# Kernel tuning notes

Measured on AMD Instinct MI355X. Metric: run time of the kernel, lower is better.

## Reference

```python
import jax, jax.numpy as jnp
import numpy as np

B, S, D, H = 2, 2048, 1024, 16
DEPTH = D // H
NEG = -1e9


def setup_inputs() -> dict:
    key = jax.random.key(0)
    ks = jax.random.split(key, 8)
    scale = 1.0 / np.sqrt(D)
    inp = {
        "query": jax.random.normal(ks[0], (B, S, D), jnp.float32),
        "key": jax.random.normal(ks[1], (B, S, D), jnp.float32),
        "value": jax.random.normal(ks[2], (B, S, D), jnp.float32),
        # causal look-ahead mask: 1 where attention is disallowed
        "mask": (1.0 - jnp.tril(jnp.ones((S, S), jnp.float32)))[None, None, :, :],
        "Wq": jax.random.normal(ks[3], (D, D), jnp.float32) * scale,
        "Wk": jax.random.normal(ks[4], (D, D), jnp.float32) * scale,
        "Wv": jax.random.normal(ks[5], (D, D), jnp.float32) * scale,
        "Wo": jax.random.normal(ks[6], (D, D), jnp.float32) * scale,
        "bq": jnp.zeros((D,), jnp.float32),
        "bk": jnp.zeros((D,), jnp.float32),
        "bv": jnp.zeros((D,), jnp.float32),
        "bo": jnp.zeros((D,), jnp.float32),
    }
    return inp


def _split_heads(x):
    # [B,S,D] -> [B,H,S,depth]
    return x.reshape(B, -1, H, DEPTH).transpose(0, 2, 1, 3)


def reference(query, key, value, mask, Wq, Wk, Wv, Wo, bq, bk, bv, bo):
    q = _split_heads(query @ Wq + bq)
    k = _split_heads(key @ Wk + bk)
    v = _split_heads(value @ Wv + bv)
    logits = jnp.einsum("bhqd,bhkd->bhqk", q, k) / jnp.sqrt(jnp.float32(DEPTH))
    logits = logits + mask * NEG
    attn = jax.nn.softmax(logits, axis=-1)
    ctx = jnp.einsum("bhqk,bhkd->bhqd", attn, v)  # [B,H,S,depth]
    concat = ctx.transpose(0, 2, 1, 3).reshape(B, -1, D)
    return concat @ Wo + bo
```

## Files before the change

kernel.cpp:

```cpp
#include <hip/hip_runtime.h>
#include <hip/hip_bf16.h>
#include <stdint.h>

#define BB 2
#define SS 2048
#define DDIM 1024
#define HH 16
#define DEPTH 64
#define MROWS (BB*SS)

typedef short bf16x8 __attribute__((ext_vector_type(8)));
typedef float f32x4 __attribute__((ext_vector_type(4)));

__device__ inline ushort f2bf(float f) {
  union { float f; unsigned u; } v; v.f = f;
  unsigned r = v.u + 0x7fffu + ((v.u >> 16) & 1u);
  return (ushort)(r >> 16);
}

__device__ inline uint pkbf(float a, float b) {
  uint r;
  asm("v_cvt_pk_bf16_f32 %0, %1, %2" : "=v"(r) : "v"(a), "v"(b));
  return r;
}

__device__ inline void gload_lds16(const void* g, void* l) {
  __builtin_amdgcn_global_load_lds(
      (const __attribute__((address_space(1))) unsigned*)g,
      (__attribute__((address_space(3))) unsigned*)l,
      16, 0, 0);
}

__global__ void wprep_kernel(const float* __restrict__ W0, const float* __restrict__ W1,
                             const float* __restrict__ W2, const float* __restrict__ W3,
                             ushort* __restrict__ T0, ushort* __restrict__ T1,
                             ushort* __restrict__ T2, ushort* __restrict__ T3) {
  __shared__ float tile[32][33];
  int z = blockIdx.x >> 10;
  int rr = blockIdx.x & 1023;
  const float* W = (z == 0) ? W0 : (z == 1) ? W1 : (z == 2) ? W2 : W3;
  ushort* T = (z == 0) ? T0 : (z == 1) ? T1 : (z == 2) ? T2 : T3;
  int tx = threadIdx.x & 31, ty = threadIdx.x >> 5;
  int n0 = (rr & 31) * 32, k0 = (rr >> 5) * 32;
#pragma unroll
  for (int i = 0; i < 4; i++)
    tile[ty + i * 8][tx] = W[(size_t)(k0 + ty + i * 8) * DDIM + n0 + tx];
  __syncthreads();
#pragma unroll
  for (int i = 0; i < 4; i++)
    T[(size_t)(n0 + ty + i * 8) * DDIM + k0 + tx] = f2bf(tile[tx][ty + i * 8]);
}

__global__ __launch_bounds__(256, 3) void qkv_gemm_kernel(
    const float* __restrict__ Aq, const float* __restrict__ Ak, const float* __restrict__ Av,
    const ushort* __restrict__ Wqt, const ushort* __restrict__ Wkt, const ushort* __restrict__ Wvt,
    const float* __restrict__ bqp, const float* __restrict__ bkp, const float* __restrict__ bvp,
    ushort* __restrict__ Qh, ushort* __restrict__ Kh, ushort* __restrict__ Vtg) {
  const int id = blockIdx.x;
  const int xcd = id & 7;
  const int rest = id >> 3;
  const int xblk = rest & 7;
  const int slot = rest >> 3;
  const int g = xcd * 12 + slot;
  const int yblk = g & 31;
  const int z = g >> 5;

  const float*  Ap = (z == 0) ? Aq  : (z == 1) ? Ak  : Av;
  const ushort* Bt = (z == 0) ? Wqt : (z == 1) ? Wkt : Wvt;
  const float* bias = (z == 0) ? bqp : (z == 1) ? bkp : bvp;

  __shared__ __align__(16) ushort As[128 * 64];
  __shared__ __align__(16) ushort Bs[128 * 64];
  const int tid = threadIdx.x;
  const int w = tid >> 6, lane = tid & 63;
  const int m0 = yblk * 128, n0 = xblk * 128;
  const int wr = (w >> 1) * 64, wc = (w & 1) * 64;
  const int l4 = lane >> 4, l15 = lane & 15;
  const int row16 = tid >> 4;
  const int col4 = (tid & 15) * 4;
  const int srow8 = w * 8 + (lane >> 3);
  const int scol8 = (lane & 7) * 8;

  f32x4 zero = {0.f, 0.f, 0.f, 0.f};
  f32x4 acc[4][4];
#pragma unroll
  for (int i = 0; i < 4; i++)
#pragma unroll
    for (int j = 0; j < 4; j++) acc[i][j] = zero;

  float4 areg[8];
#pragma unroll
  for (int j = 0; j < 8; ++j)
    areg[j] = *(const float4*)&Ap[(size_t)(m0 + j * 16 + row16) * DDIM + col4];

  for (int t = 0; t < 16; ++t) {
#pragma unroll
    for (int it = 0; it < 4; ++it)
      gload_lds16(Bt + (size_t)(n0 + it * 32 + srow8) * DDIM + t * 64 + scol8,
                  &Bs[(it * 32 + w * 8) * 64]);
#pragma unroll
    for (int j = 0; j < 8; ++j) {
      uint2 pk;
      pk.x = pkbf(areg[j].x, areg[j].y);
      pk.y = pkbf(areg[j].z, areg[j].w);
      *(uint2*)&As[(j * 16 + row16) * 64 + col4] = pk;
    }
    __syncthreads();
    if (t + 1 < 16) {
#pragma unroll
      for (int j = 0; j < 8; ++j)
        areg[j] = *(const float4*)&Ap[(size_t)(m0 + j * 16 + row16) * DDIM + (t + 1) * 64 + col4];
    }
#pragma unroll
    for (int kk = 0; kk < 2; ++kk) {
      bf16x8 af[4], bfr[4];
#pragma unroll
      for (int m = 0; m < 4; m++)
        af[m] = *(const bf16x8*)&As[(wr + m * 16 + l15) * 64 + kk * 32 + l4 * 8];
#pragma unroll
      for (int n = 0; n < 4; n++)
        bfr[n] = *(const bf16x8*)&Bs[(wc + n * 16 + l15) * 64 + kk * 32 + l4 * 8];
#pragma unroll
      for (int m = 0; m < 4; m++)
#pragma unroll
        for (int n = 0; n < 4; n++)
          acc[m][n] = __builtin_amdgcn_mfma_f32_16x16x32_bf16(af[m], bfr[n], acc[m][n], 0, 0, 0);
    }
    __syncthreads();
  }

  if (z != 2) {
    ushort* outp = (z == 0) ? Qh : Kh;
    ushort* wtile = (w < 2) ? &As[w * 4096] : &Bs[(w - 2) * 4096];
    const int gcol0 = n0 + wc;
    const int hh = gcol0 >> 6;
    const int bb = m0 >> 11;
    const int s0g = (m0 + wr) & (SS - 1);
#pragma unroll
    for (int m = 0; m < 4; m++) {
#pragma unroll
      for (int n = 0; n < 4; n++) {
        int dloc = n * 16 + l15;
        float bv = bias[gcol0 + dloc];
#pragma unroll
        for (int r = 0; r < 4; r++) {
          int sloc = m * 16 + l4 * 4 + r;
          wtile[sloc * 64 + (dloc ^ ((sloc & 7) << 3))] = f2bf(acc[m][n][r] + bv);
        }
      }
    }
#pragma unroll
    for (int i = 0; i < 8; ++i) {
      int srow = i * 8 + (lane >> 3);
      int dch = (lane & 7) * 8;
      bf16x8 val = *(const bf16x8*)&wtile[srow * 64 + (dch ^ ((srow & 7) << 3))];
      *(bf16x8*)&outp[((size_t)(bb * HH + hh) * SS + s0g + srow) * DEPTH + dch] = val;
    }
  } else {
    ushort* wtile = (w < 2) ? &As[w * 2048] : &Bs[(w - 2) * 2048];
    const int gcol0 = n0 + wc;
    const int hh = gcol0 >> 6;
    const int bb = m0 >> 11;
    const int s0g = (m0 + wr) & (SS - 1);
#pragma unroll
    for (int p = 0; p < 2; ++p) {
#pragma unroll
      for (int nn = 0; nn < 2; ++nn) {
        int n = p * 2 + nn;
        int dloc = nn * 16 + l15;
        float bv = bias[gcol0 + p * 32 + dloc];
#pragma unroll
        for (int m = 0; m < 4; m++) {
#pragma unroll
          for (int rr = 0; rr < 4; rr += 2) {
            int sloc = m * 16 + l4 * 4 + rr;
            int gg = (sloc >> 3) ^ (dloc & 7);
            uint pk = pkbf(acc[m][n][rr] + bv, acc[m][n][rr + 1] + bv);
            *(uint*)&wtile[dloc * 64 + gg * 8 + (sloc & 7)] = pk;
          }
        }
      }
      __syncthreads();
#pragma unroll
      for (int i = 0; i < 4; ++i) {
        int dloc = (lane >> 3) + i * 8;
        int gg = (lane & 7) ^ (dloc & 7);
        bf16x8 val = *(const bf16x8*)&wtile[dloc * 64 + gg * 8];
        int dglob = p * 32 + dloc;
        size_t addr = ((size_t)(bb * HH + hh) * DEPTH + dglob) * SS + s0g + (lane & 7) * 8;
        *(bf16x8*)&Vtg[addr] = val;
      }
      __syncthreads();
    }
  }
}

__global__ __launch_bounds__(256, 2) void out_gemm_kernel(
    const ushort* __restrict__ A, const ushort* __restrict__ Bt,
    const float* __restrict__ bias, float* __restrict__ out,
    int M, int N, int K) {
  __shared__ __align__(16) ushort As[128 * 64];
  __shared__ __align__(16) ushort Bs[64 * 64];
  const int id = blockIdx.x;
  const int xcd = id & 7;
  const int rest = id >> 3;
  const int xblk = rest & 15;
  const int slot = rest >> 4;
  const int yblk = xcd * 4 + slot;

  const int tid = threadIdx.x;
  const int w = tid >> 6, lane = tid & 63;
  const int m0 = yblk * 128, n0 = xblk * 64;
  const int wr = (w >> 1) * 64, wc = (w & 1) * 32;
  const int l4 = lane >> 4, l15 = lane & 15;
  const int srow8 = w * 8 + (lane >> 3);
  const int scol8 = (lane & 7) * 8;

  f32x4 zero = {0.f, 0.f, 0.f, 0.f};
  f32x4 acc[4][2];
#pragma unroll
  for (int i = 0; i < 4; i++)
#pragma unroll
    for (int j = 0; j < 2; j++) acc[i][j] = zero;

  for (int t = 0; t < 16; ++t) {
#pragma unroll
    for (int it = 0; it < 4; ++it)
      gload_lds16(A + (size_t)(m0 + it * 32 + srow8) * K + t * 64 + scol8,
                  &As[(it * 32 + w * 8) * 64]);
#pragma unroll
    for (int it = 0; it < 2; ++it)
      gload_lds16(Bt + (size_t)(n0 + it * 32 + srow8) * K + t * 64 + scol8,
                  &Bs[(it * 32 + w * 8) * 64]);
    __syncthreads();
#pragma unroll
    for (int kk = 0; kk < 2; ++kk) {
      bf16x8 af[4], bfr[2];
#pragma unroll
      for (int m = 0; m < 4; m++)
        af[m] = *(const bf16x8*)&As[(wr + m * 16 + l15) * 64 + kk * 32 + l4 * 8];
#pragma unroll
      for (int n = 0; n < 2; n++)
        bfr[n] = *(const bf16x8*)&Bs[(wc + n * 16 + l15) * 64 + kk * 32 + l4 * 8];
#pragma unroll
      for (int m = 0; m < 4; m++)
#pragma unroll
        for (int n = 0; n < 2; n++)
          acc[m][n] = __builtin_amdgcn_mfma_f32_16x16x32_bf16(af[m], bfr[n], acc[m][n], 0, 0, 0);
    }
    __syncthreads();
  }

#pragma unroll
  for (int m = 0; m < 4; m++) {
#pragma unroll
    for (int n = 0; n < 2; n++) {
      int col = n0 + wc + n * 16 + l15;
      float bv = bias[col];
#pragma unroll
      for (int r = 0; r < 4; r++) {
        int row = m0 + wr + m * 16 + l4 * 4 + r;
        out[(size_t)row * N + col] = acc[m][n][r] + bv;
      }
    }
  }
}

__global__ __launch_bounds__(256, 4) void attn_kernel(
    const ushort* __restrict__ Qh, const ushort* __restrict__ Kh,
    const ushort* __restrict__ Vt, ushort* __restrict__ ctx) {
  __shared__ __align__(16) ushort Ks[2][64 * 64];
  __shared__ __align__(16) ushort Vs[2][64 * 64];
  __shared__ __align__(16) ushort Ps[4][16 * 64];
  const int tid = threadIdx.x;
  const int w = tid >> 6, lane = tid & 63;
  const int l4 = lane >> 4, l15 = lane & 15;
  const float CE = 0.18033688f;

  const int xcd = blockIdx.x & 7;
  const int local = blockIdx.x >> 3;
  const int bh = xcd * 4 + (local & 3);
  const int chunk = 31 - (local >> 2);
  const int b = bh >> 4, h = bh & 15;
  const size_t qkbase = (size_t)bh * SS * DEPTH;
  const size_t vbase  = (size_t)bh * DEPTH * SS;

  const int srow_w = w * 8 + (lane >> 3);
  const int colb_lin = (lane & 7) * 16;
  const int swz_rd = (l15 & 7) << 3;

  const int q0 = chunk * 64 + w * 16;
  const int nt = chunk + 1;

  bf16x8 aq[2];
#pragma unroll
  for (int cc = 0; cc < 2; cc++)
    aq[cc] = *(const bf16x8*)&Qh[qkbase + (size_t)(q0 + l15) * DEPTH + cc * 32 + l4 * 8];

  f32x4 zero = {0.f, 0.f, 0.f, 0.f};
  f32x4 o[4];
  float m_run = -__builtin_inff(), l_run = 0.f;
#pragma unroll
  for (int d = 0; d < 4; d++) o[d] = zero;

  int buf = 0;
#pragma unroll
  for (int it = 0; it < 2; ++it) {
    int row = it * 32 + srow_w;
    int col_e = (colb_lin ^ ((row & 7) << 4)) >> 1;
    int ldsoff = it * 2048 + w * 512;
    gload_lds16(Kh + qkbase + (size_t)row * DEPTH + col_e, &Ks[0][ldsoff]);
    gload_lds16(Vt + vbase + (size_t)row * SS + col_e, &Vs[0][ldsoff]);
  }
  __syncthreads();

  for (int t = 0; t < nt; ++t) {
    if (t + 1 < nt) {
      const int kv1 = (t + 1) * 64;
#pragma unroll
      for (int it = 0; it < 2; ++it) {
        int row = it * 32 + srow_w;
        int col_e = (colb_lin ^ ((row & 7) << 4)) >> 1;
        int ldsoff = it * 2048 + w * 512;
        gload_lds16(Kh + qkbase + (size_t)(kv1 + row) * DEPTH + col_e, &Ks[buf ^ 1][ldsoff]);
        gload_lds16(Vt + vbase + (size_t)row * SS + kv1 + col_e, &Vs[buf ^ 1][ldsoff]);
      }
    }

    const int kv0 = t * 64;
    f32x4 s[4];
    __builtin_amdgcn_s_setprio(1);
#pragma unroll
    for (int n = 0; n < 4; n++) {
      f32x4 zacc = zero;
      int kr = n * 16 + l15;
#pragma unroll
      for (int cc = 0; cc < 2; cc++) {
        bf16x8 bk = *(const bf16x8*)&Ks[buf][kr * 64 + ((cc * 32 + l4 * 8) ^ swz_rd)];
        zacc = __builtin_amdgcn_mfma_f32_16x16x32_bf16(bk, aq[cc], zacc, 0, 0, 0);
      }
      s[n] = zacc;
    }
    __builtin_amdgcn_s_setprio(0);

    const int qg = q0 + l15;
    if (t == nt - 1) {
#pragma unroll
      for (int n = 0; n < 4; n++) {
        int kb = kv0 + n * 16 + l4 * 4;
#pragma unroll
        for (int r = 0; r < 4; r++)
          if (kb + r > qg) s[n][r] = -1e9f;
      }
    }

    float mx = -__builtin_inff();
#pragma unroll
    for (int n = 0; n < 4; n++)
      mx = fmaxf(mx, fmaxf(fmaxf(s[n][0], s[n][1]), fmaxf(s[n][2], s[n][3])));
    mx = fmaxf(mx, __shfl_xor(mx, 16));
    mx = fmaxf(mx, __shfl_xor(mx, 32));
    if (!__all(mx - m_run <= 44.36f)) {
      float mnew = fmaxf(m_run, mx);
      float alpha = exp2f((m_run - mnew) * CE);
      m_run = mnew;
      l_run *= alpha;
#pragma unroll
      for (int d = 0; d < 4; d++) o[d] *= alpha;
    }
    float mc = m_run * CE;
    float rs = 0.f;
#pragma unroll
    for (int n = 0; n < 4; n++)
#pragma unroll
      for (int r = 0; r < 4; r++) {
        float p = exp2f(s[n][r] * CE - mc);
        s[n][r] = p;
        rs += p;
      }
    l_run += rs;

    ushort* Pw = &Ps[w][0];
#pragma unroll
    for (int n = 0; n < 4; n++) {
      int col = (n * 16 + l4 * 4) ^ swz_rd;
      *(uint*)&Pw[l15 * 64 + col]     = pkbf(s[n][0], s[n][1]);
      *(uint*)&Pw[l15 * 64 + col + 2] = pkbf(s[n][2], s[n][3]);
    }

    bf16x8 pa[2];
#pragma unroll
    for (int cc = 0; cc < 2; cc++)
      pa[cc] = *(const bf16x8*)&Pw[l15 * 64 + ((cc * 32 + l4 * 8) ^ swz_rd)];

    __builtin_amdgcn_s_setprio(1);
#pragma unroll
    for (int d = 0; d < 4; d++) {
      int dr = d * 16 + l15;
#pragma unroll
      for (int cc = 0; cc < 2; cc++) {
        bf16x8 av = *(const bf16x8*)&Vs[buf][dr * 64 + ((cc * 32 + l4 * 8) ^ swz_rd)];
        o[d] = __builtin_amdgcn_mfma_f32_16x16x32_bf16(av, pa[cc], o[d], 0, 0, 0);
      }
    }
    __builtin_amdgcn_s_setprio(0);

    __syncthreads();
    buf ^= 1;
  }

  float lv = l_run;
  lv += __shfl_xor(lv, 16);
  lv += __shfl_xor(lv, 32);
  float inv = 1.f / lv;
  size_t rowbase = ((size_t)(b * SS + q0 + l15)) * DDIM + h * DEPTH;
#pragma unroll
  for (int d = 0; d < 4; d++) {
    *(uint*)&ctx[rowbase + d * 16 + l4 * 4]     = pkbf(o[d][0] * inv, o[d][1] * inv);
    *(uint*)&ctx[rowbase + d * 16 + l4 * 4 + 2] = pkbf(o[d][2] * inv, o[d][3] * inv);
  }
}

extern "C" void kernel_launch(void* const* d_in, const int* in_sizes, int n_in,
                              void* d_out, int out_size, void* d_ws, size_t ws_size,
                              hipStream_t stream) {
  const float* query = (const float*)d_in[0];
  const float* key_  = (const float*)d_in[1];
  const float* value = (const float*)d_in[2];
  const float* Wq = (const float*)d_in[4];
  const float* Wk = (const float*)d_in[5];
  const float* Wv = (const float*)d_in[6];
  const float* Wo = (const float*)d_in[7];
  const float* bq = (const float*)d_in[8];
  const float* bk = (const float*)d_in[9];
  const float* bv = (const float*)d_in[10];
  const float* bo = (const float*)d_in[11];

  char* ws = (char*)d_ws;
  const size_t MB = 1u << 20;
  ushort* Wqt = (ushort*)(ws + 24 * MB);
  ushort* Wkt = (ushort*)(ws + 26 * MB);
  ushort* Wvt = (ushort*)(ws + 28 * MB);
  ushort* Wot = (ushort*)(ws + 30 * MB);
  ushort* Qh  = (ushort*)(ws + 32 * MB);
  ushort* Kh  = (ushort*)(ws + 40 * MB);
  ushort* Vtg = (ushort*)(ws + 48 * MB);
  ushort* Cb  = (ushort*)(ws + 56 * MB);

  wprep_kernel<<<4096, 256, 0, stream>>>(Wq, Wk, Wv, Wo, Wqt, Wkt, Wvt, Wot);

  qkv_gemm_kernel<<<768, 256, 0, stream>>>(
      query, key_, value, Wqt, Wkt, Wvt, bq, bk, bv, Qh, Kh, Vtg);

  attn_kernel<<<1024, 256, 0, stream>>>(Qh, Kh, Vtg, Cb);

  out_gemm_kernel<<<512, 256, 0, stream>>>(
      Cb, Wot, bo, (float*)d_out, MROWS, DDIM, DDIM);
}
```

Measured before the change: 118.2 us.

## Double-buffer LDS tiles in QKV and output GEMMs to overlap loads with MFMA

The QKV projection GEMM and the output GEMM now double-buffer their B (and, for the output GEMM, A) shared-memory tiles. The next K-slice is issued with async global-to-LDS loads before the MFMA work on the current slice, which is meant to hide global load latency behind compute. The output GEMM's launch bound is raised to 3 blocks per CU. The attention kernel also merges two 32-bit P stores into one 64-bit store. The trade-off is more LDS per block, which may limit occupancy. In the QKV kernel the A tile is still single-buffered, so a second barrier per iteration remains.

New measurement: 116.8 us. Within noise of the previous version (-1.1%).

```diff
diff --git a/kernel.cpp b/kernel.cpp
--- a/kernel.cpp
+++ b/kernel.cpp
@@ -70,7 +70,7 @@
   const float* bias = (z == 0) ? bqp : (z == 1) ? bkp : bvp;
 
   __shared__ __align__(16) ushort As[128 * 64];
-  __shared__ __align__(16) ushort Bs[128 * 64];
+  __shared__ __align__(16) ushort Bs[2][128 * 64];
   const int tid = threadIdx.x;
   const int w = tid >> 6, lane = tid & 63;
   const int m0 = yblk * 128, n0 = xblk * 128;
@@ -92,46 +92,62 @@
 #pragma unroll
   for (int j = 0; j < 8; ++j)
     areg[j] = *(const float4*)&Ap[(size_t)(m0 + j * 16 + row16) * DDIM + col4];
-
+#pragma unroll
+  for (int it = 0; it < 4; ++it)
+    gload_lds16(Bt + (size_t)(n0 + it * 32 + srow8) * DDIM + scol8,
+                &Bs[0][(it * 32 + w * 8) * 64]);
+#pragma unroll
+  for (int j = 0; j < 8; ++j) {
+    uint2 pk;
+    pk.x = pkbf(areg[j].x, areg[j].y);
+    pk.y = pkbf(areg[j].z, areg[j].w);
+    *(uint2*)&As[(j * 16 + row16) * 64 + col4] = pk;
+  }
+  __syncthreads();
+
+  int buf = 0;
   for (int t = 0; t < 16; ++t) {
-#pragma unroll
-    for (int it = 0; it < 4; ++it)
-      gload_lds16(Bt + (size_t)(n0 + it * 32 + srow8) * DDIM + t * 64 + scol8,
-                  &Bs[(it * 32 + w * 8) * 64]);
-#pragma unroll
-    for (int j = 0; j < 8; ++j) {
-      uint2 pk;
-      pk.x = pkbf(areg[j].x, areg[j].y);
-      pk.y = pkbf(areg[j].z, areg[j].w);
-      *(uint2*)&As[(j * 16 + row16) * 64 + col4] = pk;
+    if (t + 1 < 16) {
+#pragma unroll
+      for (int it = 0; it < 4; ++it)
+        gload_lds16(Bt + (size_t)(n0 + it * 32 + srow8) * DDIM + (t + 1) * 64 + scol8,
+                    &Bs[buf ^ 1][(it * 32 + w * 8) * 64]);
+#pragma unroll
+      for (int j = 0; j < 8; ++j)
+        areg[j] = *(const float4*)&Ap[(size_t)(m0 + j * 16 + row16) * DDIM + (t + 1) * 64 + col4];
+    }
+#pragma unroll
+    for (int kk = 0; kk < 2; ++kk) {
+      bf16x8 af[4], bfr[4];
+#pragma unroll
+      for (int m = 0; m < 4; m++)
+        af[m] = *(const bf16x8*)&As[(wr + m * 16 + l15) * 64 + kk * 32 + l4 * 8];
+#pragma unroll
+      for (int n = 0; n < 4; n++)
+        bfr[n] = *(const bf16x8*)&Bs[buf][(wc + n * 16 + l15) * 64 + kk * 32 + l4 * 8];
+#pragma unroll
+      for (int m = 0; m < 4; m++)
+#pragma unroll
+        for (int n = 0; n < 4; n++)
+          acc[m][n] = __builtin_amdgcn_mfma_f32_16x16x32_bf16(af[m], bfr[n], acc[m][n], 0, 0, 0);
     }
     __syncthreads();
     if (t + 1 < 16) {
 #pragma unroll
-      for (int j = 0; j < 8; ++j)
-        areg[j] = *(const float4*)&Ap[(size_t)(m0 + j * 16 + row16) * DDIM + (t + 1) * 64 + col4];
-    }
-#pragma unroll
-    for (int kk = 0; kk < 2; ++kk) {
-      bf16x8 af[4], bfr[4];
-#pragma unroll
-      for (int m = 0; m < 4; m++)
-        af[m] = *(const bf16x8*)&As[(wr + m * 16 + l15) * 64 + kk * 32 + l4 * 8];
-#pragma unroll
-      for (int n = 0; n < 4; n++)
-        bfr[n] = *(const bf16x8*)&Bs[(wc + n * 16 + l15) * 64 + kk * 32 + l4 * 8];
-#pragma unroll
-      for (int m = 0; m < 4; m++)
-#pragma unroll
-        for (int n = 0; n < 4; n++)
-          acc[m][n] = __builtin_amdgcn_mfma_f32_16x16x32_bf16(af[m], bfr[n], acc[m][n], 0, 0, 0);
+      for (int j = 0; j < 8; ++j) {
+        uint2 pk;
+        pk.x = pkbf(areg[j].x, areg[j].y);
+        pk.y = pkbf(areg[j].z, areg[j].w);
+        *(uint2*)&As[(j * 16 + row16) * 64 + col4] = pk;
+      }
     }
     __syncthreads();
+    buf ^= 1;
   }
 
   if (z != 2) {
     ushort* outp = (z == 0) ? Qh : Kh;
-    ushort* wtile = (w < 2) ? &As[w * 4096] : &Bs[(w - 2) * 4096];
+    ushort* wtile = (w < 2) ? &As[w * 4096] : &Bs[0][(w - 2) * 4096];
     const int gcol0 = n0 + wc;
     const int hh = gcol0 >> 6;
     const int bb = m0 >> 11;
@@ -157,7 +173,7 @@
       *(bf16x8*)&outp[((size_t)(bb * HH + hh) * SS + s0g + srow) * DEPTH + dch] = val;
     }
   } else {
-    ushort* wtile = (w < 2) ? &As[w * 2048] : &Bs[(w - 2) * 2048];
+    ushort* wtile = (w < 2) ? &As[w * 2048] : &Bs[0][(w - 2) * 2048];
     const int gcol0 = n0 + wc;
     const int hh = gcol0 >> 6;
     const int bb = m0 >> 11;
@@ -195,12 +211,12 @@
   }
 }
 
-__global__ __launch_bounds__(256, 2) void out_gemm_kernel(
+__global__ __launch_bounds__(256, 3) void out_gemm_kernel(
     const ushort* __restrict__ A, const ushort* __restrict__ Bt,
     const float* __restrict__ bias, float* __restrict__ out,
     int M, int N, int K) {
-  __shared__ __align__(16) ushort As[128 * 64];
-  __shared__ __align__(16) ushort Bs[64 * 64];
+  __shared__ __align__(16) ushort As[2][128 * 64];
+  __shared__ __align__(16) ushort Bs[2][64 * 64];
   const int id = blockIdx.x;
   const int xcd = id & 7;
   const int rest = id >> 3;
@@ -223,25 +239,37 @@
 #pragma unroll
     for (int j = 0; j < 2; j++) acc[i][j] = zero;
 
+#pragma unroll
+  for (int it = 0; it < 4; ++it)
+    gload_lds16(A + (size_t)(m0 + it * 32 + srow8) * K + scol8,
+                &As[0][(it * 32 + w * 8) * 64]);
+#pragma unroll
+  for (int it = 0; it < 2; ++it)
+    gload_lds16(Bt + (size_t)(n0 + it * 32 + srow8) * K + scol8,
+                &Bs[0][(it * 32 + w * 8) * 64]);
+  __syncthreads();
+
+  int buf = 0;
   for (int t = 0; t < 16; ++t) {
-#pragma unroll
-    for (int it = 0; it < 4; ++it)
-      gload_lds16(A + (size_t)(m0 + it * 32 + srow8) * K + t * 64 + scol8,
-                  &As[(it * 32 + w * 8) * 64]);
-#pragma unroll
-    for (int it = 0; it < 2; ++it)
-      gload_lds16(Bt + (size_t)(n0 + it * 32 + srow8) * K + t * 64 + scol8,
-                  &Bs[(it * 32 + w * 8) * 64]);
-    __syncthreads();
+    if (t + 1 < 16) {
+#pragma unroll
+      for (int it = 0; it < 4; ++it)
+        gload_lds16(A + (size_t)(m0 + it * 32 + srow8) * K + (t + 1) * 64 + scol8,
+                    &As[buf ^ 1][(it * 32 + w * 8) * 64]);
+#pragma unroll
+      for (int it = 0; it < 2; ++it)
+        gload_lds16(Bt + (size_t)(n0 + it * 32 + srow8) * K + (t + 1) * 64 + scol8,
+                    &Bs[buf ^ 1][(it * 32 + w * 8) * 64]);
+    }
 #pragma unroll
     for (int kk = 0; kk < 2; ++kk) {
       bf16x8 af[4], bfr[2];
 #pragma unroll
       for (int m = 0; m < 4; m++)
-        af[m] = *(const bf16x8*)&As[(wr + m * 16 + l15) * 64 + kk * 32 + l4 * 8];
+        af[m] = *(const bf16x8*)&As[buf][(wr + m * 16 + l15) * 64 + kk * 32 + l4 * 8];
 #pragma unroll
       for (int n = 0; n < 2; n++)
-        bfr[n] = *(const bf16x8*)&Bs[(wc + n * 16 + l15) * 64 + kk * 32 + l4 * 8];
+        bfr[n] = *(const bf16x8*)&Bs[buf][(wc + n * 16 + l15) * 64 + kk * 32 + l4 * 8];
 #pragma unroll
       for (int m = 0; m < 4; m++)
 #pragma unroll
@@ -249,6 +277,7 @@
           acc[m][n] = __builtin_amdgcn_mfma_f32_16x16x32_bf16(af[m], bfr[n], acc[m][n], 0, 0, 0);
     }
     __syncthreads();
+    buf ^= 1;
   }
 
 #pragma unroll
@@ -384,8 +413,10 @@
 #pragma unroll
     for (int n = 0; n < 4; n++) {
       int col = (n * 16 + l4 * 4) ^ swz_rd;
-      *(uint*)&Pw[l15 * 64 + col]     = pkbf(s[n][0], s[n][1]);
-      *(uint*)&Pw[l15 * 64 + col + 2] = pkbf(s[n][2], s[n][3]);
+      uint2 pk;
+      pk.x = pkbf(s[n][0], s[n][1]);
+      pk.y = pkbf(s[n][2], s[n][3]);
+      *(uint2*)&Pw[l15 * 64 + col] = pk;
     }
 
     bf16x8 pa[2];
```
